# Performance work log

Measured on AMD Instinct MI355X. Metric: run time of the kernel, lower is better.

## Reference

```python
import jax, jax.numpy as jnp
import numpy as np

NHEAD = 8
NPTS = 4

def _bilinear_sample(E_flat, locs, H, W):
    # E_flat: [B, H*W, D] channel-last flattened feature map
    # locs:   [B, N, 2] normalized (x, y) in [-1, 1], align_corners=False, zeros padding
    ix = ((locs[..., 0] + 1.0) * W - 1.0) * 0.5
    iy = ((locs[..., 1] + 1.0) * H - 1.0) * 0.5
    x0 = jnp.floor(ix); y0 = jnp.floor(iy)
    x1 = x0 + 1.0;      y1 = y0 + 1.0
    wx1 = ix - x0; wx0 = 1.0 - wx1
    wy1 = iy - y0; wy0 = 1.0 - wy1
    gather = jax.vmap(lambda e, i: e[i])  # per-batch gather -> [B, N, D]
    def corner(xc, yc, w):
        valid = (xc >= 0) & (xc < W) & (yc >= 0) & (yc < H)
        xi = jnp.clip(xc, 0, W - 1).astype(jnp.int32)
        yi = jnp.clip(yc, 0, H - 1).astype(jnp.int32)
        g = gather(E_flat, yi * W + xi)
        return g * (w * valid)[..., None]
    return (corner(x0, y0, wx0 * wy0) + corner(x1, y0, wx1 * wy0)
            + corner(x0, y1, wx0 * wy1) + corner(x1, y1, wx1 * wy1))

def setup_inputs() -> dict:
    key = jax.random.key(0)
    ks = jax.random.split(key, 6)
    B, M, D = 8, 1024, 256
    H, Wd = 100, 100
    SADQ = jax.random.normal(ks[0], (B, M, D), jnp.float32)
    E = jax.random.normal(ks[1], (B, H * Wd, D), jnp.float32)
    # learned params (random instead of the degenerate zero-init, so the math is exercised)
    Wo = jax.random.normal(ks[2], (D, NHEAD * NPTS * 2), jnp.float32) * 0.02
    bo = jnp.zeros((NHEAD * NPTS * 2,), jnp.float32)
    Wa = jax.random.normal(ks[3], (D, NHEAD * NPTS), jnp.float32) * 0.05
    ba = jnp.zeros((NHEAD * NPTS,), jnp.float32)
    Wr = jax.random.normal(ks[4], (D, 2), jnp.float32) * 0.05
    br = jnp.zeros((2,), jnp.float32)
    Wp = jax.random.normal(ks[5], (D, D), jnp.float32) * 0.05
    bp = jnp.zeros((D,), jnp.float32)
    return {"SADQ": SADQ, "E": E, "Wo": Wo, "bo": bo, "Wa": Wa, "ba": ba,
            "Wr": Wr, "br": br, "Wp": Wp, "bp": bp, "H": H, "W": Wd}

def reference(SADQ, E, Wo, bo, Wa, ba, Wr, br, Wp, bp, H, W):
    B, M, D = SADQ.shape
    offsets = (SADQ @ Wo + bo).reshape(B, M, NHEAD, NPTS, 2)
    attn = jax.nn.softmax((SADQ @ Wa + ba).reshape(B, M, NHEAD, NPTS), axis=-1)
    base_ref = (SADQ @ Wr + br)[:, :, None, None, :]            # [B, M, 1, 1, 2]
    locs = (base_ref + offsets * 0.1).reshape(B, M * NHEAD * NPTS, 2)
    sampled = _bilinear_sample(E, locs, H, W).reshape(B, M, NHEAD, NPTS, D)
    # sum over points, mean over heads, fused into one contraction
    agg = jnp.einsum('bmhpd,bmhp->bmd', sampled, attn) / NHEAD
    return agg @ Wp + bp
```

## Files before the change

kernel.cpp:

```cpp
#include <hip/hip_runtime.h>
#include <hip/hip_bf16.h>
#include <math.h>

#define BATCH 8
#define MQ    1024
#define DIM   256
#define NHEAD 8
#define NPTS  4
#define NPROJ 98
#define PSTR  112

typedef __attribute__((ext_vector_type(8))) short  short8;
typedef __attribute__((ext_vector_type(4))) float  f32x4;

static __device__ __forceinline__ ushort f2bf(float f) {
    union { float f; unsigned u; } v; v.f = f;
    const unsigned r = v.u + 0x7fffu + ((v.u >> 16) & 1u);
    return (ushort)(r >> 16);
}

#define KEEP4(v) asm volatile("" : "+v"(v.x), "+v"(v.y), "+v"(v.z), "+v"(v.w))

__global__ __launch_bounds__(112) void wcat_build_kernel(
    const float* __restrict__ Wo, const float* __restrict__ bo,
    const float* __restrict__ Wa, const float* __restrict__ ba,
    const float* __restrict__ Wr, const float* __restrict__ br,
    float* __restrict__ Wcat, float* __restrict__ bcat)
{
    const int k = blockIdx.x;
    const int j = threadIdx.x;
    float w = 0.f, bias = 0.f;
    if (j < 64)      { w = Wo[k * 64 + j];        bias = bo[j]; }
    else if (j < 96) { w = Wa[k * 32 + (j - 64)]; bias = ba[j - 64]; }
    else if (j < 98) { w = Wr[k * 2  + (j - 96)]; bias = br[j - 96]; }
    Wcat[k * PSTR + j] = w;
    if (k == 0) bcat[j] = bias;
}

__global__ __launch_bounds__(256) void proj_kernel(
    const float* __restrict__ SADQ,
    const float* __restrict__ Wcat,
    const float* __restrict__ bcat,
    float* __restrict__ P)
{
    __shared__ float Qs[32][65];
    __shared__ float Ws[64][112];

    const int tid  = threadIdx.x;
    const int row0 = blockIdx.x * 32;
    const int rg   = tid >> 4;
    const int cg   = tid & 15;

    float acc0[7] = {};
    float acc1[7] = {};

    for (int kc = 0; kc < DIM; kc += 64) {
        #pragma unroll
        for (int i = 0; i < 2; ++i) {
            const int fi = tid * 2 + i;
            const int r  = fi >> 4;
            const int k4 = (fi & 15) * 4;
            const float4 v = *(const float4*)&SADQ[(size_t)(row0 + r) * DIM + kc + k4];
            Qs[r][k4 + 0] = v.x; Qs[r][k4 + 1] = v.y;
            Qs[r][k4 + 2] = v.z; Qs[r][k4 + 3] = v.w;
        }
        for (int fi = tid; fi < 64 * 28; fi += 256) {
            const int k  = fi / 28;
            const int j4 = (fi % 28) * 4;
            *(float4*)&Ws[k][j4] = *(const float4*)&Wcat[(size_t)(kc + k) * PSTR + j4];
        }
        __syncthreads();

        #pragma unroll 8
        for (int k = 0; k < 64; ++k) {
            const float q0 = Qs[rg * 2 + 0][k];
            const float q1 = Qs[rg * 2 + 1][k];
            #pragma unroll
            for (int j = 0; j < 7; ++j) {
                const float w = Ws[k][cg * 7 + j];
                acc0[j] = fmaf(q0, w, acc0[j]);
                acc1[j] = fmaf(q1, w, acc1[j]);
            }
        }
        __syncthreads();
    }

    #pragma unroll
    for (int j = 0; j < 7; ++j) {
        const int col = cg * 7 + j;
        const float bb = bcat[col];
        P[(size_t)(row0 + rg * 2 + 0) * PSTR + col] = acc0[j] + bb;
        P[(size_t)(row0 + rg * 2 + 1) * PSTR + col] = acc1[j] + bb;
    }
}

__global__ __launch_bounds__(256) void gather_kernel(
    const float* __restrict__ P,
    const float* __restrict__ E,
    const int*   __restrict__ Hp, const int* __restrict__ Wdp,
    ushort* __restrict__ aggb)
{
    const int tid  = threadIdx.x;
    const int wid  = tid >> 6;
    const int lane = tid & 63;
    const int row  = blockIdx.x * 4 + wid;
    const int b    = row >> 10;

    __shared__ float sW[4][128];
    __shared__ int   sIdx[4][128];

    const int Hh = *Hp;
    const int Ww = *Wdp;

    if (lane < 32) {
        const int p = lane;
        const float* Pr = P + (size_t)row * PSTR;
        const float lg = Pr[64 + p];
        float mx = fmaxf(lg, __shfl_xor(lg, 1));
        mx = fmaxf(mx, __shfl_xor(mx, 2));
        const float e = expf(lg - mx);
        float s = e + __shfl_xor(e, 1);
        s += __shfl_xor(s, 2);
        const float aw = e / s * (1.f / NHEAD);

        const float lx = Pr[96] + 0.1f * Pr[p * 2 + 0];
        const float ly = Pr[97] + 0.1f * Pr[p * 2 + 1];
        const float ix = ((lx + 1.f) * (float)Ww - 1.f) * 0.5f;
        const float iy = ((ly + 1.f) * (float)Hh - 1.f) * 0.5f;
        const float x0f = floorf(ix), y0f = floorf(iy);
        const int   x0  = (int)x0f,   y0  = (int)y0f;
        const float wx1 = ix - x0f, wx0 = 1.f - wx1;
        const float wy1 = iy - y0f, wy0 = 1.f - wy1;

        #pragma unroll
        for (int c = 0; c < 4; ++c) {
            const int   xc = x0 + (c & 1);
            const int   yc = y0 + (c >> 1);
            const float wx = (c & 1) ? wx1 : wx0;
            const float wy = (c >> 1) ? wy1 : wy0;
            const bool valid = (xc >= 0) && (xc < Ww) && (yc >= 0) && (yc < Hh);
            const int xi = min(max(xc, 0), Ww - 1);
            const int yi = min(max(yc, 0), Hh - 1);
            sW  [wid][p * 4 + c] = valid ? (wx * wy * aw) : 0.f;
            sIdx[wid][p * 4 + c] = (yi * Ww + xi) * (DIM / 4);
        }
    }
    __syncthreads();

    const float4* __restrict__ Eb4 =
        (const float4*)(E + (size_t)b * (size_t)(Hh * Ww) * DIM);

    float4 acc = make_float4(0.f, 0.f, 0.f, 0.f);
    for (int t = 0; t < 128; t += 8) {
        const float w0 = sW[wid][t + 0]; const int i0 = sIdx[wid][t + 0];
        const float w1 = sW[wid][t + 1]; const int i1 = sIdx[wid][t + 1];
        const float w2 = sW[wid][t + 2]; const int i2 = sIdx[wid][t + 2];
        const float w3 = sW[wid][t + 3]; const int i3 = sIdx[wid][t + 3];
        const float w4 = sW[wid][t + 4]; const int i4 = sIdx[wid][t + 4];
        const float w5 = sW[wid][t + 5]; const int i5 = sIdx[wid][t + 5];
        const float w6 = sW[wid][t + 6]; const int i6 = sIdx[wid][t + 6];
        const float w7 = sW[wid][t + 7]; const int i7 = sIdx[wid][t + 7];

        float4 e0 = Eb4[(size_t)i0 + lane];
        float4 e1 = Eb4[(size_t)i1 + lane];
        float4 e2 = Eb4[(size_t)i2 + lane];
        float4 e3 = Eb4[(size_t)i3 + lane];
        float4 e4 = Eb4[(size_t)i4 + lane];
        float4 e5 = Eb4[(size_t)i5 + lane];
        float4 e6 = Eb4[(size_t)i6 + lane];
        float4 e7 = Eb4[(size_t)i7 + lane];
        KEEP4(e0); KEEP4(e1); KEEP4(e2); KEEP4(e3);
        KEEP4(e4); KEEP4(e5); KEEP4(e6); KEEP4(e7);

        acc.x = fmaf(w0, e0.x, acc.x); acc.y = fmaf(w0, e0.y, acc.y);
        acc.z = fmaf(w0, e0.z, acc.z); acc.w = fmaf(w0, e0.w, acc.w);
        acc.x = fmaf(w1, e1.x, acc.x); acc.y = fmaf(w1, e1.y, acc.y);
        acc.z = fmaf(w1, e1.z, acc.z); acc.w = fmaf(w1, e1.w, acc.w);
        acc.x = fmaf(w2, e2.x, acc.x); acc.y = fmaf(w2, e2.y, acc.y);
        acc.z = fmaf(w2, e2.z, acc.z); acc.w = fmaf(w2, e2.w, acc.w);
        acc.x = fmaf(w3, e3.x, acc.x); acc.y = fmaf(w3, e3.y, acc.y);
        acc.z = fmaf(w3, e3.z, acc.z); acc.w = fmaf(w3, e3.w, acc.w);
        acc.x = fmaf(w4, e4.x, acc.x); acc.y = fmaf(w4, e4.y, acc.y);
        acc.z = fmaf(w4, e4.z, acc.z); acc.w = fmaf(w4, e4.w, acc.w);
        acc.x = fmaf(w5, e5.x, acc.x); acc.y = fmaf(w5, e5.y, acc.y);
        acc.z = fmaf(w5, e5.z, acc.z); acc.w = fmaf(w5, e5.w, acc.w);
        acc.x = fmaf(w6, e6.x, acc.x); acc.y = fmaf(w6, e6.y, acc.y);
        acc.z = fmaf(w6, e6.z, acc.z); acc.w = fmaf(w6, e6.w, acc.w);
        acc.x = fmaf(w7, e7.x, acc.x); acc.y = fmaf(w7, e7.y, acc.y);
        acc.z = fmaf(w7, e7.z, acc.z); acc.w = fmaf(w7, e7.w, acc.w);
    }

    ushort4 o;
    o.x = f2bf(acc.x); o.y = f2bf(acc.y);
    o.z = f2bf(acc.z); o.w = f2bf(acc.w);
    *(ushort4*)&aggb[(size_t)row * DIM + lane * 4] = o;
}

__global__ __launch_bounds__(256) void wp_convert_kernel(
    const float* __restrict__ Wp, ushort* __restrict__ WpT)
{
    const int k = blockIdx.x;
    const int n = threadIdx.x;
    WpT[(size_t)n * DIM + k] = f2bf(Wp[(size_t)k * DIM + n]);
}

__global__ __launch_bounds__(256) void mfma_gemm_kernel(
    const ushort* __restrict__ A,
    const ushort* __restrict__ BT,
    const float*  __restrict__ bp,
    float* __restrict__ out)
{
    __shared__ ushort ldsA[64 * 40];
    __shared__ ushort ldsB[64 * 40];

    const int tid  = threadIdx.x;
    const int mb   = blockIdx.x * 64;
    const int nb   = blockIdx.y * 64;
    const int wave = tid >> 6;
    const int lane = tid & 63;
    const int r0   = (wave >> 1) * 32;
    const int c0   = (wave & 1) * 32;
    const int lrow = lane & 15;
    const int kgrp = lane >> 4;

    const int sm = tid >> 2;
    const int sc = (tid & 3) * 8;

    f32x4 acc00 = {0.f, 0.f, 0.f, 0.f};
    f32x4 acc01 = {0.f, 0.f, 0.f, 0.f};
    f32x4 acc10 = {0.f, 0.f, 0.f, 0.f};
    f32x4 acc11 = {0.f, 0.f, 0.f, 0.f};

    for (int kb = 0; kb < DIM; kb += 32) {
        *(uint4*)&ldsA[sm * 40 + sc] =
            *(const uint4*)&A[(size_t)(mb + sm) * DIM + kb + sc];
        *(uint4*)&ldsB[sm * 40 + sc] =
            *(const uint4*)&BT[(size_t)(nb + sm) * DIM + kb + sc];
        __syncthreads();

        const short8 a0 = *(const short8*)&ldsA[(r0 + lrow)      * 40 + kgrp * 8];
        const short8 a1 = *(const short8*)&ldsA[(r0 + 16 + lrow) * 40 + kgrp * 8];
        const short8 b0 = *(const short8*)&ldsB[(c0 + lrow)      * 40 + kgrp * 8];
        const short8 b1 = *(const short8*)&ldsB[(c0 + 16 + lrow) * 40 + kgrp * 8];

        acc00 = __builtin_amdgcn_mfma_f32_16x16x32_bf16(a0, b0, acc00, 0, 0, 0);
        acc01 = __builtin_amdgcn_mfma_f32_16x16x32_bf16(a0, b1, acc01, 0, 0, 0);
        acc10 = __builtin_amdgcn_mfma_f32_16x16x32_bf16(a1, b0, acc10, 0, 0, 0);
        acc11 = __builtin_amdgcn_mfma_f32_16x16x32_bf16(a1, b1, acc11, 0, 0, 0);
        __syncthreads();
    }

    const int orow = mb + r0 + kgrp * 4;
    const int ocol = nb + c0 + lrow;
    const float bp0 = bp[ocol];
    const float bp1 = bp[ocol + 16];
    #pragma unroll
    for (int reg = 0; reg < 4; ++reg) {
        out[(size_t)(orow + reg)      * DIM + ocol]      = acc00[reg] + bp0;
        out[(size_t)(orow + reg)      * DIM + ocol + 16] = acc01[reg] + bp1;
        out[(size_t)(orow + 16 + reg) * DIM + ocol]      = acc10[reg] + bp0;
        out[(size_t)(orow + 16 + reg) * DIM + ocol + 16] = acc11[reg] + bp1;
    }
}

extern "C" void kernel_launch(void* const* d_in, const int* in_sizes, int n_in,
                              void* d_out, int out_size, void* d_ws, size_t ws_size,
                              hipStream_t stream)
{
    const float* SADQ = (const float*)d_in[0];
    const float* E    = (const float*)d_in[1];
    const float* Wo   = (const float*)d_in[2];
    const float* bo   = (const float*)d_in[3];
    const float* Wa   = (const float*)d_in[4];
    const float* ba   = (const float*)d_in[5];
    const float* Wr   = (const float*)d_in[6];
    const float* br   = (const float*)d_in[7];
    const float* Wp   = (const float*)d_in[8];
    const float* bp   = (const float*)d_in[9];
    const int*   Hp   = (const int*)d_in[10];
    const int*   Wdp  = (const int*)d_in[11];

    const int BM = in_sizes[0] / DIM;

    char* ws = (char*)d_ws;
    ushort* aggb = (ushort*)(ws);
    ushort* WpT  = (ushort*)(ws + 4194304);
    float*  P    = (float*) (ws + 4194304 + 131072);
    float*  Wcat = (float*) (ws + 4194304 + 131072 + 3670016);
    float*  bcat = (float*) (ws + 4194304 + 131072 + 3670016 + 114688);
    float*  out  = (float*)d_out;

    wcat_build_kernel<<<DIM, PSTR, 0, stream>>>(Wo, bo, Wa, ba, Wr, br, Wcat, bcat);
    proj_kernel<<<BM / 32, 256, 0, stream>>>(SADQ, Wcat, bcat, P);
    gather_kernel<<<BM / 4, 256, 0, stream>>>(P, E, Hp, Wdp, aggb);
    wp_convert_kernel<<<DIM, 256, 0, stream>>>(Wp, WpT);

    dim3 g2(BM / 64, DIM / 64);
    mfma_gemm_kernel<<<g2, 256, 0, stream>>>(aggb, WpT, bp, out);
}
```

Measured before the change: 217.3 us.

## Shrink projection tiles and remap gather blocks so each XCD handles one batch

The projection kernel now computes 16 rows per block instead of 32, with a 32-wide K chunk and one row per thread, so the launch has twice as many blocks. The gather kernel permutes its block index so that consecutive blocks scheduled round-robin across the 8 XCDs all work on the same batch. Each batch's feature map is then more likely to stay resident in one XCD's L2. The smaller projection tile reuses each loaded Wcat element less per block and adds more synchronisation per unit of work.

```diff
diff --git a/kernel.cpp b/kernel.cpp
--- a/kernel.cpp
+++ b/kernel.cpp
@@ -43,28 +43,25 @@
     const float* __restrict__ bcat,
     float* __restrict__ P)
 {
-    __shared__ float Qs[32][65];
-    __shared__ float Ws[64][112];
+    __shared__ float Qs[16][36];
+    __shared__ float Ws[32][112];
 
     const int tid  = threadIdx.x;
-    const int row0 = blockIdx.x * 32;
+    const int row0 = blockIdx.x * 16;
     const int rg   = tid >> 4;
     const int cg   = tid & 15;
 
-    float acc0[7] = {};
-    float acc1[7] = {};
-
-    for (int kc = 0; kc < DIM; kc += 64) {
-        #pragma unroll
-        for (int i = 0; i < 2; ++i) {
-            const int fi = tid * 2 + i;
-            const int r  = fi >> 4;
-            const int k4 = (fi & 15) * 4;
+    float acc[7] = {};
+
+    for (int kc = 0; kc < DIM; kc += 32) {
+        if (tid < 128) {
+            const int r  = tid >> 3;
+            const int k4 = (tid & 7) * 4;
             const float4 v = *(const float4*)&SADQ[(size_t)(row0 + r) * DIM + kc + k4];
             Qs[r][k4 + 0] = v.x; Qs[r][k4 + 1] = v.y;
             Qs[r][k4 + 2] = v.z; Qs[r][k4 + 3] = v.w;
         }
-        for (int fi = tid; fi < 64 * 28; fi += 256) {
+        for (int fi = tid; fi < 32 * 28; fi += 256) {
             const int k  = fi / 28;
             const int j4 = (fi % 28) * 4;
             *(float4*)&Ws[k][j4] = *(const float4*)&Wcat[(size_t)(kc + k) * PSTR + j4];
@@ -72,15 +69,11 @@
         __syncthreads();
 
         #pragma unroll 8
-        for (int k = 0; k < 64; ++k) {
-            const float q0 = Qs[rg * 2 + 0][k];
-            const float q1 = Qs[rg * 2 + 1][k];
+        for (int k = 0; k < 32; ++k) {
+            const float q = Qs[rg][k];
             #pragma unroll
-            for (int j = 0; j < 7; ++j) {
-                const float w = Ws[k][cg * 7 + j];
-                acc0[j] = fmaf(q0, w, acc0[j]);
-                acc1[j] = fmaf(q1, w, acc1[j]);
-            }
+            for (int j = 0; j < 7; ++j)
+                acc[j] = fmaf(q, Ws[k][cg * 7 + j], acc[j]);
         }
         __syncthreads();
     }
@@ -88,9 +81,7 @@
     #pragma unroll
     for (int j = 0; j < 7; ++j) {
         const int col = cg * 7 + j;
-        const float bb = bcat[col];
-        P[(size_t)(row0 + rg * 2 + 0) * PSTR + col] = acc0[j] + bb;
-        P[(size_t)(row0 + rg * 2 + 1) * PSTR + col] = acc1[j] + bb;
+        P[(size_t)(row0 + rg) * PSTR + col] = acc[j] + bcat[col];
     }
 }
 
@@ -103,7 +94,10 @@
     const int tid  = threadIdx.x;
     const int wid  = tid >> 6;
     const int lane = tid & 63;
-    const int row  = blockIdx.x * 4 + wid;
+    const int bid  = blockIdx.x;
+    const int cpx  = (int)(gridDim.x >> 3);
+    const int sb   = (bid & 7) * cpx + (bid >> 3);
+    const int row  = sb * 4 + wid;
     const int b    = row >> 10;
 
     __shared__ float sW[4][128];
@@ -291,7 +285,7 @@
     float*  out  = (float*)d_out;
 
     wcat_build_kernel<<<DIM, PSTR, 0, stream>>>(Wo, bo, Wa, ba, Wr, br, Wcat, bcat);
-    proj_kernel<<<BM / 32, 256, 0, stream>>>(SADQ, Wcat, bcat, P);
+    proj_kernel<<<BM / 16, 256, 0, stream>>>(SADQ, Wcat, bcat, P);
     gather_kernel<<<BM / 4, 256, 0, stream>>>(P, E, Hp, Wdp, aggb);
     wp_convert_kernel<<<DIM, 256, 0, stream>>>(Wp, WpT);
 
```

New measurement: 226.2 us. 1.04x slower.
